# Optimization experiments

Measured on AMD Instinct MI355X. Metric: run time of the kernel, lower is better.

Reference implementation:

```python
import jax, jax.numpy as jnp
import numpy as np

B, S, D, H = 4, 2048, 1024, 16
DK = D // H  # 64

def setup_inputs() -> dict:
    key = jax.random.key(0)
    kq, kk, kv = jax.random.split(key, 3)
    q = jax.random.normal(kq, (B, S, D), dtype=jnp.float32)
    k = jax.random.normal(kk, (B, S, D), dtype=jnp.float32)
    v = jax.random.normal(kv, (B, S, D), dtype=jnp.float32)
    return {"q": q, "k": k, "v": v}

def reference(q, k, v):
    # [B,S,D] -> [B,H,S,DK]
    qh = q.reshape(B, S, H, DK).transpose(0, 2, 1, 3)
    kh = k.reshape(B, S, H, DK).transpose(0, 2, 1, 3)
    vh = v.reshape(B, S, H, DK).transpose(0, 2, 1, 3)
    scale = 1.0 / np.sqrt(DK).astype(np.float32)
    scores = jnp.einsum('bhqd,bhkd->bhqk', qh, kh) * scale  # [B,H,S,S]
    probs = jax.nn.softmax(scores, axis=-1)
    out = jnp.einsum('bhqk,bhkd->bhqd', probs, vh)  # [B,H,S,DK]
    # concat heads: [B,S,D]
    return out.transpose(0, 2, 1, 3).reshape(B, S, D)
```

## Files before the change

kernel.cpp:

```cpp
#include <hip/hip_runtime.h>

#define B_   4
#define S_   2048
#define D_   1024
#define H_   16
#define DKV  64
#define BM   128
#define BN   64
#define NT   (S_ / BN)
#define PITCH 72

typedef float f32x4 __attribute__((ext_vector_type(4)));
typedef short bf16x8 __attribute__((ext_vector_type(8)));
typedef unsigned short ushort8_t __attribute__((ext_vector_type(8)));

__device__ __forceinline__ unsigned short f2b(float f) {
  union { float f; unsigned int u; } x; x.f = f;
  unsigned int u = x.u;
  unsigned int r = u + 0x7FFFu + ((u >> 16) & 1u);
  return (unsigned short)(r >> 16);
}

__global__ __launch_bounds__(256)
void prep_kv_kernel(const float* __restrict__ k, const float* __restrict__ v,
                    unsigned short* __restrict__ kb, unsigned short* __restrict__ vt) {
  __shared__ unsigned int sT[64 * 33];
  const int tid = threadIdx.x;
  const int s0  = blockIdx.x * 64;
  const int bh  = blockIdx.y;
  const int b   = bh >> 4;
  const int h   = bh & 15;

  for (int it = 0; it < 4; ++it) {
    int id  = tid + it * 256;
    int r   = id >> 4;
    int c4  = (id & 15) << 2;
    const size_t goff = ((size_t)(b * S_ + s0 + r)) * D_ + h * DKV + c4;
    const float4 fk = *reinterpret_cast<const float4*>(k + goff);
    unsigned k01, k23;
    asm("v_cvt_pk_bf16_f32 %0, %1, %2" : "=v"(k01) : "v"(fk.x), "v"(fk.y));
    asm("v_cvt_pk_bf16_f32 %0, %1, %2" : "=v"(k23) : "v"(fk.z), "v"(fk.w));
    uint2 uk; uk.x = k01; uk.y = k23;
    *reinterpret_cast<uint2*>(kb + goff) = uk;

    const float4 fv = *reinterpret_cast<const float4*>(v + goff);
    unsigned v01, v23;
    asm("v_cvt_pk_bf16_f32 %0, %1, %2" : "=v"(v01) : "v"(fv.x), "v"(fv.y));
    asm("v_cvt_pk_bf16_f32 %0, %1, %2" : "=v"(v23) : "v"(fv.z), "v"(fv.w));
    sT[r * 33 + (c4 >> 1)]     = v01;
    sT[r * 33 + (c4 >> 1) + 1] = v23;
  }
  __syncthreads();
  const unsigned short* sTs = reinterpret_cast<const unsigned short*>(sT);
  for (int it = 0; it < 2; ++it) {
    int id = tid + it * 256;
    int d  = id >> 3;
    int s8 = (id & 7) << 3;
    ushort8_t u;
    for (int t = 0; t < 8; ++t) u[t] = sTs[(s8 + t) * 66 + d];
    *reinterpret_cast<ushort8_t*>(vt + ((size_t)(bh * DKV + d)) * S_ + s0 + s8) = u;
  }
}

__global__ __launch_bounds__(256, 4)
void mha_fast_kernel(const float* __restrict__ q,
                     const unsigned short* __restrict__ kb,
                     const unsigned short* __restrict__ vt,
                     float* __restrict__ out) {
  __shared__ __align__(16) unsigned short sK [2][BN  * PITCH];
  __shared__ __align__(16) unsigned short sVt[2][DKV * PITCH];

  const int tid  = threadIdx.x;
  const int wave = tid >> 6;
  const int lane = tid & 63;
  const int ln   = lane & 15;
  const int quad = lane >> 4;

  const int bh = blockIdx.y;
  const int b  = bh >> 4;
  const int h  = bh & 15;
  const int q0 = blockIdx.x * BM;

  const float* qg = q + (size_t)b * S_ * D_ + h * DKV;
  const unsigned short* kbase = kb + (size_t)b * S_ * D_ + h * DKV;
  const unsigned short* vbase = vt + (size_t)bh * DKV * S_;
  float* og = out + (size_t)b * S_ * D_ + h * DKV;

  const float qs = 0.125f * 1.44269504088896340736f;

  bf16x8 qf[2][2];
  for (int mt = 0; mt < 2; ++mt)
    for (int ks = 0; ks < 2; ++ks) {
      const float* base = qg + (size_t)(q0 + wave * 32 + mt * 16 + ln) * D_
                             + ks * 32 + quad * 8;
      const float4 f0 = *reinterpret_cast<const float4*>(base);
      const float4 f1 = *reinterpret_cast<const float4*>(base + 4);
      bf16x8 a;
      a[0] = (short)f2b(f0.x * qs); a[1] = (short)f2b(f0.y * qs);
      a[2] = (short)f2b(f0.z * qs); a[3] = (short)f2b(f0.w * qs);
      a[4] = (short)f2b(f1.x * qs); a[5] = (short)f2b(f1.y * qs);
      a[6] = (short)f2b(f1.z * qs); a[7] = (short)f2b(f1.w * qs);
      qf[mt][ks] = a;
    }

  float l_part[2] = {0.f, 0.f};
  f32x4 o[2][4];
  for (int mt = 0; mt < 2; ++mt)
    for (int dt = 0; dt < 4; ++dt) o[mt][dt] = (f32x4){0.f, 0.f, 0.f, 0.f};

  int n_[2], c8_[2];
  for (int it = 0; it < 2; ++it) {
    int id = tid + it * 256;
    n_[it]  = id >> 3;
    c8_[it] = (id & 7) << 3;
  }

  ushort8_t pk[2], pv[2];
  for (int it = 0; it < 2; ++it) {
    pk[it] = *reinterpret_cast<const ushort8_t*>(kbase + (size_t)n_[it] * D_ + c8_[it]);
    pv[it] = *reinterpret_cast<const ushort8_t*>(vbase + (size_t)n_[it] * S_ + c8_[it]);
  }
  for (int it = 0; it < 2; ++it) {
    *reinterpret_cast<ushort8_t*>(&sK [0][n_[it] * PITCH + c8_[it]]) = pk[it];
    *reinterpret_cast<ushort8_t*>(&sVt[0][n_[it] * PITCH + c8_[it]]) = pv[it];
  }
  for (int it = 0; it < 2; ++it) {
    pk[it] = *reinterpret_cast<const ushort8_t*>(kbase + (size_t)(BN + n_[it]) * D_ + c8_[it]);
    pv[it] = *reinterpret_cast<const ushort8_t*>(vbase + (size_t)n_[it] * S_ + BN + c8_[it]);
  }
  __syncthreads();

  for (int i = 0; i < NT; ++i) {
    const int cur = i & 1;

    if (i + 1 < NT) {
      for (int it = 0; it < 2; ++it) {
        *reinterpret_cast<ushort8_t*>(&sK [cur ^ 1][n_[it] * PITCH + c8_[it]]) = pk[it];
        *reinterpret_cast<ushort8_t*>(&sVt[cur ^ 1][n_[it] * PITCH + c8_[it]]) = pv[it];
      }
    }
    if (i + 2 < NT) {
      const int nn = (i + 2) * BN;
      for (int it = 0; it < 2; ++it) {
        pk[it] = *reinterpret_cast<const ushort8_t*>(
            kbase + (size_t)(nn + n_[it]) * D_ + c8_[it]);
        pv[it] = *reinterpret_cast<const ushort8_t*>(
            vbase + (size_t)n_[it] * S_ + nn + c8_[it]);
      }
    }

    const unsigned short* sKc = sK [cur];
    const unsigned short* sVc = sVt[cur];

    bf16x8 pA[2][2];
    for (int g = 0; g < 2; ++g) {
      unsigned lo[2][2], hi[2][2];
      for (int t = 0; t < 2; ++t) {
        const int nt = g * 2 + t;
        bf16x8 kf0 = *reinterpret_cast<const bf16x8*>(&sKc[(nt * 16 + ln) * PITCH + quad * 8]);
        bf16x8 kf1 = *reinterpret_cast<const bf16x8*>(&sKc[(nt * 16 + ln) * PITCH + 32 + quad * 8]);
        for (int mt = 0; mt < 2; ++mt) {
          f32x4 acc = (f32x4){0.f, 0.f, 0.f, 0.f};
          acc = __builtin_amdgcn_mfma_f32_16x16x32_bf16(kf0, qf[mt][0], acc, 0, 0, 0);
          acc = __builtin_amdgcn_mfma_f32_16x16x32_bf16(kf1, qf[mt][1], acc, 0, 0, 0);
          float p0 = __builtin_amdgcn_exp2f(acc[0]);
          float p1 = __builtin_amdgcn_exp2f(acc[1]);
          float p2 = __builtin_amdgcn_exp2f(acc[2]);
          float p3 = __builtin_amdgcn_exp2f(acc[3]);
          l_part[mt] += (p0 + p1) + (p2 + p3);
          unsigned plo, phi;
          asm("v_cvt_pk_bf16_f32 %0, %1, %2" : "=v"(plo) : "v"(p0), "v"(p1));
          asm("v_cvt_pk_bf16_f32 %0, %1, %2" : "=v"(phi) : "v"(p2), "v"(p3));
          lo[mt][t] = plo; hi[mt][t] = phi;
        }
      }
      for (int mt = 0; mt < 2; ++mt) {
        unsigned x = lo[mt][0], y = lo[mt][1];
        asm("v_permlane32_swap_b32 %0, %1" : "+v"(x), "+v"(y));
        asm("v_permlane16_swap_b32 %0, %1" : "+v"(x), "+v"(y));
        unsigned u = hi[mt][0], w = hi[mt][1];
        asm("v_permlane32_swap_b32 %0, %1" : "+v"(u), "+v"(w));
        asm("v_permlane16_swap_b32 %0, %1" : "+v"(u), "+v"(w));
        union { unsigned u32[4]; bf16x8 v8; } pw;
        pw.u32[0] = x; pw.u32[1] = u; pw.u32[2] = y; pw.u32[3] = w;
        pA[mt][g] = pw.v8;
      }
    }

    __builtin_amdgcn_s_setprio(1);
    for (int g = 0; g < 2; ++g) {
      for (int dt = 0; dt < 4; ++dt) {
        bf16x8 vf = *reinterpret_cast<const bf16x8*>(
            &sVc[(dt * 16 + ln) * PITCH + g * 32 + quad * 8]);
        for (int mt = 0; mt < 2; ++mt)
          o[mt][dt] = __builtin_amdgcn_mfma_f32_16x16x32_bf16(pA[mt][g], vf, o[mt][dt], 0, 0, 0);
      }
    }
    __builtin_amdgcn_s_setprio(0);

    __syncthreads();
  }

  for (int mt = 0; mt < 2; ++mt) {
    float l = l_part[mt];
    l += __shfl_xor(l, 16, 64);
    l += __shfl_xor(l, 32, 64);
    const float linv = 1.f / l;
    float invr[4];
    for (int r = 0; r < 4; ++r)
      invr[r] = __shfl(linv, quad * 4 + r, 64);
    float* orow = og + (size_t)(q0 + wave * 32 + mt * 16 + quad * 4) * D_;
    for (int r = 0; r < 4; ++r)
      for (int dt = 0; dt < 4; ++dt)
        orow[(size_t)r * D_ + dt * 16 + ln] = o[mt][dt][r] * invr[r];
  }
}

extern "C" void kernel_launch(void* const* d_in, const int* in_sizes, int n_in,
                              void* d_out, int out_size, void* d_ws, size_t ws_size,
                              hipStream_t stream) {
  const float* q = (const float*)d_in[0];
  const float* k = (const float*)d_in[1];
  const float* v = (const float*)d_in[2];
  float* out = (float*)d_out;

  unsigned short* kb = (unsigned short*)d_ws;
  unsigned short* vt = kb + (size_t)B_ * S_ * D_;

  prep_kv_kernel<<<dim3(S_ / 64, B_ * H_), dim3(256), 0, stream>>>(k, v, kb, vt);
  mha_fast_kernel<<<dim3(S_ / BM, B_ * H_), dim3(256), 0, stream>>>(q, kb, vt, out);
}
```

Measured before the change: 212.3 us.

## Process two KV tiles per barrier epoch and swap grid dimensions

The main loop now loads both shared-memory buffers with consecutive K/V tiles, then computes on both within one epoch. This replaces the per-tile double-buffer ping-pong and halves the number of loop iterations, at the cost of two barriers per epoch and twice as many prefetch registers. The grid is also transposed so that consecutive blocks cover different heads at the same query tile, which changes L2 locality of the shared K/V reads. The s_setprio hints around the PV MFMA block are removed.

```diff
diff --git a/kernel.cpp b/kernel.cpp
--- a/kernel.cpp
+++ b/kernel.cpp
@@ -7,7 +7,7 @@
 #define DKV  64
 #define BM   128
 #define BN   64
-#define NT   (S_ / BN)
+#define NE   (S_ / (2 * BN))
 #define PITCH 72
 
 typedef float f32x4 __attribute__((ext_vector_type(4)));
@@ -76,10 +76,10 @@
   const int ln   = lane & 15;
   const int quad = lane >> 4;
 
-  const int bh = blockIdx.y;
+  const int bh = blockIdx.x;
   const int b  = bh >> 4;
   const int h  = bh & 15;
-  const int q0 = blockIdx.x * BM;
+  const int q0 = blockIdx.y * BM;
 
   const float* qg = q + (size_t)b * S_ * D_ + h * DKV;
   const unsigned short* kbase = kb + (size_t)b * S_ * D_ + h * DKV;
@@ -115,90 +115,84 @@
     c8_[it] = (id & 7) << 3;
   }
 
-  ushort8_t pk[2], pv[2];
-  for (int it = 0; it < 2; ++it) {
-    pk[it] = *reinterpret_cast<const ushort8_t*>(kbase + (size_t)n_[it] * D_ + c8_[it]);
-    pv[it] = *reinterpret_cast<const ushort8_t*>(vbase + (size_t)n_[it] * S_ + c8_[it]);
-  }
-  for (int it = 0; it < 2; ++it) {
-    *reinterpret_cast<ushort8_t*>(&sK [0][n_[it] * PITCH + c8_[it]]) = pk[it];
-    *reinterpret_cast<ushort8_t*>(&sVt[0][n_[it] * PITCH + c8_[it]]) = pv[it];
-  }
-  for (int it = 0; it < 2; ++it) {
-    pk[it] = *reinterpret_cast<const ushort8_t*>(kbase + (size_t)(BN + n_[it]) * D_ + c8_[it]);
-    pv[it] = *reinterpret_cast<const ushort8_t*>(vbase + (size_t)n_[it] * S_ + BN + c8_[it]);
-  }
-  __syncthreads();
-
-  for (int i = 0; i < NT; ++i) {
-    const int cur = i & 1;
-
-    if (i + 1 < NT) {
+  ushort8_t pk[2][2], pv[2][2];
+  for (int hf = 0; hf < 2; ++hf)
+    for (int it = 0; it < 2; ++it) {
+      pk[hf][it] = *reinterpret_cast<const ushort8_t*>(
+          kbase + (size_t)(hf * BN + n_[it]) * D_ + c8_[it]);
+      pv[hf][it] = *reinterpret_cast<const ushort8_t*>(
+          vbase + (size_t)n_[it] * S_ + hf * BN + c8_[it]);
+    }
+
+  for (int e = 0; e < NE; ++e) {
+    __syncthreads();
+
+    for (int hf = 0; hf < 2; ++hf)
       for (int it = 0; it < 2; ++it) {
-        *reinterpret_cast<ushort8_t*>(&sK [cur ^ 1][n_[it] * PITCH + c8_[it]]) = pk[it];
-        *reinterpret_cast<ushort8_t*>(&sVt[cur ^ 1][n_[it] * PITCH + c8_[it]]) = pv[it];
+        *reinterpret_cast<ushort8_t*>(&sK [hf][n_[it] * PITCH + c8_[it]]) = pk[hf][it];
+        *reinterpret_cast<ushort8_t*>(&sVt[hf][n_[it] * PITCH + c8_[it]]) = pv[hf][it];
       }
-    }
-    if (i + 2 < NT) {
-      const int nn = (i + 2) * BN;
-      for (int it = 0; it < 2; ++it) {
-        pk[it] = *reinterpret_cast<const ushort8_t*>(
-            kbase + (size_t)(nn + n_[it]) * D_ + c8_[it]);
-        pv[it] = *reinterpret_cast<const ushort8_t*>(
-            vbase + (size_t)n_[it] * S_ + nn + c8_[it]);
+    __syncthreads();
+
+    if (e + 1 < NE) {
+      const int nn = (e + 1) * 2 * BN;
+      for (int hf = 0; hf < 2; ++hf)
+        for (int it = 0; it < 2; ++it) {
+          pk[hf][it] = *reinterpret_cast<const ushort8_t*>(
+              kbase + (size_t)(nn + hf * BN + n_[it]) * D_ + c8_[it]);
+          pv[hf][it] = *reinterpret_cast<const ushort8_t*>(
+              vbase + (size_t)n_[it] * S_ + nn + hf * BN + c8_[it]);
+        }
+    }
+
+    for (int hf = 0; hf < 2; ++hf) {
+      const unsigned short* sKc = sK [hf];
+      const unsigned short* sVc = sVt[hf];
+
+      bf16x8 pA[2][2];
+      for (int g = 0; g < 2; ++g) {
+        unsigned lo[2][2], hi[2][2];
+        for (int t = 0; t < 2; ++t) {
+          const int nt = g * 2 + t;
+          bf16x8 kf0 = *reinterpret_cast<const bf16x8*>(&sKc[(nt * 16 + ln) * PITCH + quad * 8]);
+          bf16x8 kf1 = *reinterpret_cast<const bf16x8*>(&sKc[(nt * 16 + ln) * PITCH + 32 + quad * 8]);
+          for (int mt = 0; mt < 2; ++mt) {
+            f32x4 acc = (f32x4){0.f, 0.f, 0.f, 0.f};
+            acc = __builtin_amdgcn_mfma_f32_16x16x32_bf16(kf0, qf[mt][0], acc, 0, 0, 0);
+            acc = __builtin_amdgcn_mfma_f32_16x16x32_bf16(kf1, qf[mt][1], acc, 0, 0, 0);
+            float p0 = __builtin_amdgcn_exp2f(acc[0]);
+            float p1 = __builtin_amdgcn_exp2f(acc[1]);
+            float p2 = __builtin_amdgcn_exp2f(acc[2]);
+            float p3 = __builtin_amdgcn_exp2f(acc[3]);
+            l_part[mt] += (p0 + p1) + (p2 + p3);
+            unsigned plo, phi;
+            asm("v_cvt_pk_bf16_f32 %0, %1, %2" : "=v"(plo) : "v"(p0), "v"(p1));
+            asm("v_cvt_pk_bf16_f32 %0, %1, %2" : "=v"(phi) : "v"(p2), "v"(p3));
+            lo[mt][t] = plo; hi[mt][t] = phi;
+          }
+        }
+        for (int mt = 0; mt < 2; ++mt) {
+          unsigned x = lo[mt][0], y = lo[mt][1];
+          asm("v_permlane32_swap_b32 %0, %1" : "+v"(x), "+v"(y));
+          asm("v_permlane16_swap_b32 %0, %1" : "+v"(x), "+v"(y));
+          unsigned u = hi[mt][0], w = hi[mt][1];
+          asm("v_permlane32_swap_b32 %0, %1" : "+v"(u), "+v"(w));
+          asm("v_permlane16_swap_b32 %0, %1" : "+v"(u), "+v"(w));
+          union { unsigned u32[4]; bf16x8 v8; } pw;
+          pw.u32[0] = x; pw.u32[1] = u; pw.u32[2] = y; pw.u32[3] = w;
+          pA[mt][g] = pw.v8;
+        }
       }
-    }
-
-    const unsigned short* sKc = sK [cur];
-    const unsigned short* sVc = sVt[cur];
-
-    bf16x8 pA[2][2];
-    for (int g = 0; g < 2; ++g) {
-      unsigned lo[2][2], hi[2][2];
-      for (int t = 0; t < 2; ++t) {
-        const int nt = g * 2 + t;
-        bf16x8 kf0 = *reinterpret_cast<const bf16x8*>(&sKc[(nt * 16 + ln) * PITCH + quad * 8]);
-        bf16x8 kf1 = *reinterpret_cast<const bf16x8*>(&sKc[(nt * 16 + ln) * PITCH + 32 + quad * 8]);
-        for (int mt = 0; mt < 2; ++mt) {
-          f32x4 acc = (f32x4){0.f, 0.f, 0.f, 0.f};
-          acc = __builtin_amdgcn_mfma_f32_16x16x32_bf16(kf0, qf[mt][0], acc, 0, 0, 0);
-          acc = __builtin_amdgcn_mfma_f32_16x16x32_bf16(kf1, qf[mt][1], acc, 0, 0, 0);
-          float p0 = __builtin_amdgcn_exp2f(acc[0]);
-          float p1 = __builtin_amdgcn_exp2f(acc[1]);
-          float p2 = __builtin_amdgcn_exp2f(acc[2]);
-          float p3 = __builtin_amdgcn_exp2f(acc[3]);
-          l_part[mt] += (p0 + p1) + (p2 + p3);
-          unsigned plo, phi;
-          asm("v_cvt_pk_bf16_f32 %0, %1, %2" : "=v"(plo) : "v"(p0), "v"(p1));
-          asm("v_cvt_pk_bf16_f32 %0, %1, %2" : "=v"(phi) : "v"(p2), "v"(p3));
-          lo[mt][t] = plo; hi[mt][t] = phi;
+
+      for (int g = 0; g < 2; ++g) {
+        for (int dt = 0; dt < 4; ++dt) {
+          bf16x8 vf = *reinterpret_cast<const bf16x8*>(
+              &sVc[(dt * 16 + ln) * PITCH + g * 32 + quad * 8]);
+          for (int mt = 0; mt < 2; ++mt)
+            o[mt][dt] = __builtin_amdgcn_mfma_f32_16x16x32_bf16(pA[mt][g], vf, o[mt][dt], 0, 0, 0);
         }
       }
-      for (int mt = 0; mt < 2; ++mt) {
-        unsigned x = lo[mt][0], y = lo[mt][1];
-        asm("v_permlane32_swap_b32 %0, %1" : "+v"(x), "+v"(y));
-        asm("v_permlane16_swap_b32 %0, %1" : "+v"(x), "+v"(y));
-        unsigned u = hi[mt][0], w = hi[mt][1];
-        asm("v_permlane32_swap_b32 %0, %1" : "+v"(u), "+v"(w));
-        asm("v_permlane16_swap_b32 %0, %1" : "+v"(u), "+v"(w));
-        union { unsigned u32[4]; bf16x8 v8; } pw;
-        pw.u32[0] = x; pw.u32[1] = u; pw.u32[2] = y; pw.u32[3] = w;
-        pA[mt][g] = pw.v8;
-      }
-    }
-
-    __builtin_amdgcn_s_setprio(1);
-    for (int g = 0; g < 2; ++g) {
-      for (int dt = 0; dt < 4; ++dt) {
-        bf16x8 vf = *reinterpret_cast<const bf16x8*>(
-            &sVc[(dt * 16 + ln) * PITCH + g * 32 + quad * 8]);
-        for (int mt = 0; mt < 2; ++mt)
-          o[mt][dt] = __builtin_amdgcn_mfma_f32_16x16x32_bf16(pA[mt][g], vf, o[mt][dt], 0, 0, 0);
-      }
-    }
-    __builtin_amdgcn_s_setprio(0);
-
-    __syncthreads();
+    }
   }
 
   for (int mt = 0; mt < 2; ++mt) {
@@ -228,5 +222,5 @@
   unsigned short* vt = kb + (size_t)B_ * S_ * D_;
 
   prep_kv_kernel<<<dim3(S_ / 64, B_ * H_), dim3(256), 0, stream>>>(k, v, kb, vt);
-  mha_fast_kernel<<<dim3(S_ / BM, B_ * H_), dim3(256), 0, stream>>>(q, kb, vt, out);
-}
+  mha_fast_kernel<<<dim3(B_ * H_, S_ / BM), dim3(256), 0, stream>>>(q, kb, vt, out);
+}
```

Result: slower. 328.7 us (+54.8%).
